# Optimization experiments

Hardware: AMD Instinct MI355X
Metric: run time of the kernel (lower is better)

The kernel has to match this reference:

```python
import jax, jax.numpy as jnp
import numpy as np

SEM_ENC_DIM = 1024
SENT_HIDDEN_DIM = 1024
ATT_DIM = 512

def setup_inputs() -> dict:
    key = jax.random.key(0)
    ks = jax.random.split(key, 8)
    B, L = 64, 2048
    s = lambda d: 1.0 / np.sqrt(d)
    return {
        "sem_enc_output": jax.random.normal(ks[0], (B, L, SEM_ENC_DIM), dtype=jnp.float32),
        "dec_hidden_state": jax.random.normal(ks[1], (B, SENT_HIDDEN_DIM), dtype=jnp.float32),
        "W_enc": jax.random.uniform(ks[2], (SEM_ENC_DIM, ATT_DIM), jnp.float32, -s(SEM_ENC_DIM), s(SEM_ENC_DIM)),
        "b_enc": jax.random.uniform(ks[3], (ATT_DIM,), jnp.float32, -s(SEM_ENC_DIM), s(SEM_ENC_DIM)),
        "W_dec": jax.random.uniform(ks[4], (SENT_HIDDEN_DIM, ATT_DIM), jnp.float32, -s(SENT_HIDDEN_DIM), s(SENT_HIDDEN_DIM)),
        "b_dec": jax.random.uniform(ks[5], (ATT_DIM,), jnp.float32, -s(SENT_HIDDEN_DIM), s(SENT_HIDDEN_DIM)),
        "W_full": jax.random.uniform(ks[6], (ATT_DIM, 1), jnp.float32, -s(ATT_DIM), s(ATT_DIM)),
        "b_full": jax.random.uniform(ks[7], (1,), jnp.float32, -s(ATT_DIM), s(ATT_DIM)),
    }

def reference(sem_enc_output, dec_hidden_state, W_enc, b_enc, W_dec, b_dec, W_full, b_full):
    # enc projection: [B, L, att_dim]
    enc_proj = jnp.einsum('ble,ea->bla', sem_enc_output, W_enc) + b_enc
    # dec projection: [B, att_dim]
    dec_proj = dec_hidden_state @ W_dec + b_dec
    # broadcast add + tanh: [B, L, att_dim]
    joined = jnp.tanh(enc_proj + dec_proj[:, None, :])
    # scoring: [B, L]
    scores = (jnp.einsum('bla,a->bl', joined, W_full[:, 0]) + b_full[0])
    att_scores = jax.nn.softmax(scores, axis=1)
    # weighted sum over L of the PROJECTED encoder output (matches torch code)
    att_output = jnp.einsum('bl,bla->ba', att_scores, enc_proj)
    return (att_output, att_scores)
```

## Files before the change

### kernel.cpp

```cpp
#include <hip/hip_runtime.h>
#include <hip/hip_bf16.h>
#include <cstdint>
#include <cstddef>

#define BB   64
#define LL   2048
#define ED   1024
#define AD   512
#define BM   128
#define NCH  (LL / BM)
#define NBURST 8

typedef short  short8  __attribute__((ext_vector_type(8)));
typedef float  f32x4   __attribute__((ext_vector_type(4)));

__device__ __forceinline__ unsigned short f2bf(float x) {
  unsigned u = __float_as_uint(x);
  u += 0x7FFFu + ((u >> 16) & 1u);
  return (unsigned short)(u >> 16);
}

__device__ __forceinline__ short8 cvt8(f32x4 lo, f32x4 hi) {
  union { short8 s; unsigned u[4]; } r;
  asm("v_cvt_pk_bf16_f32 %0, %1, %2" : "=v"(r.u[0]) : "v"(lo[0]), "v"(lo[1]));
  asm("v_cvt_pk_bf16_f32 %0, %1, %2" : "=v"(r.u[1]) : "v"(lo[2]), "v"(lo[3]));
  asm("v_cvt_pk_bf16_f32 %0, %1, %2" : "=v"(r.u[2]) : "v"(hi[0]), "v"(hi[1]));
  asm("v_cvt_pk_bf16_f32 %0, %1, %2" : "=v"(r.u[3]) : "v"(hi[2]), "v"(hi[3]));
  return r.s;
}

#define GLOAD_LDS16(gp, lp)                                                        \
  __builtin_amdgcn_global_load_lds(                                                \
      (const __attribute__((address_space(1))) unsigned int*)(gp),                 \
      (__attribute__((address_space(3))) unsigned int*)(lp), 16, 0, 0)

__global__ __launch_bounds__(512) void prep_kernel(
    const float* __restrict__ W_enc, const float* __restrict__ dec,
    const float* __restrict__ W_dec, const float* __restrict__ b_dec,
    unsigned short* __restrict__ Wb, float* __restrict__ dp) {
  const int blk = blockIdx.x, t = threadIdx.x;
  if (blk < BB) {
    const float* drow = dec + blk * ED;
    float a0 = 0.f, a1 = 0.f, a2 = 0.f, a3 = 0.f;
    for (int k = 0; k < ED; k += 4) {
      a0 = fmaf(drow[k],     W_dec[(k)     * AD + t], a0);
      a1 = fmaf(drow[k + 1], W_dec[(k + 1) * AD + t], a1);
      a2 = fmaf(drow[k + 2], W_dec[(k + 2) * AD + t], a2);
      a3 = fmaf(drow[k + 3], W_dec[(k + 3) * AD + t], a3);
    }
    dp[blk * AD + t] = (a0 + a1) + (a2 + a3) + b_dec[t];
  } else {
    const int base = (blk - BB) * 4096;
#pragma unroll
    for (int ii = 0; ii < 8; ii++) {
      const int o    = base + ii * 512 + t;
      const int ks   = o >> 14;
      const int cblk = (o >> 9) & 31;
      const int kg   = (o >> 7) & 3;
      const int r    = (o >> 3) & 15;
      const int j    = o & 7;
      const int k    = ks * 32 + kg * 8 + j;
      const int c    = cblk * 16 + r;
      Wb[o] = f2bf(W_enc[k * AD + c]);
    }
  }
}

__global__ __launch_bounds__(512, 2) void fused_kernel(
    const float* __restrict__ sem, const unsigned short* __restrict__ Wb,
    const float* __restrict__ dp, const float* __restrict__ b_enc,
    const float* __restrict__ Wf,
    float* __restrict__ raw_scores,
    float* __restrict__ ws_ms, float* __restrict__ ws_o) {

  __shared__ float Alds[2][16384];

  const int t    = threadIdx.x;
  const int lane = t & 63;
  const int wave = t >> 6;
  const int wm   = wave >> 2;
  const int wn   = wave & 3;
  const int b    = blockIdx.y;
  const int chunk= blockIdx.x;
  const int l0   = chunk * BM;

  const int trow = t >> 5;
  const int su   = (t & 31) ^ (trow & 7);
  const float* asrc = sem + ((size_t)(b * LL + l0 + trow)) * ED + su * 4;

  const int arow = lane & 15;
  const int akg  = lane >> 4;
  const int lxor = lane & 7;
  const int akg2 = akg * 2;
  const int arbase = (wm * 64 + arow) * 128;

  const unsigned short* wbbase = Wb + wn * 4096 + lane * 8;

  f32x4 acc[4][8];
#pragma unroll
  for (int i = 0; i < 4; i++)
#pragma unroll
    for (int j = 0; j < 8; j++) acc[i][j] = (f32x4)0.f;

#define STAGE_A(g, nb)                                                             \
  _Pragma("unroll")                                                                \
  for (int j = 0; j < 8; j++)                                                      \
    GLOAD_LDS16(asrc + (size_t)j * 16384 + (g) * 128, &Alds[nb][j * 2048 + t * 4]);

  STAGE_A(0, 0);
  asm volatile("s_waitcnt vmcnt(0)" ::: "memory");
  __builtin_amdgcn_sched_barrier(0);
  __builtin_amdgcn_s_barrier();

  for (int g = 0; g < NBURST; g++) {
    const int cb = g & 1;
    if (g + 1 < NBURST) STAGE_A(g + 1, cb ^ 1);
    __builtin_amdgcn_sched_barrier(0);
    const unsigned short* wbg = wbbase + g * 65536;
#pragma unroll
    for (int ks4 = 0; ks4 < 4; ks4++) {
      short8 bv[8];
#pragma unroll
      for (int nf = 0; nf < 8; nf++)
        bv[nf] = *(const short8*)(wbg + ks4 * 16384 + nf * 512);
      short8 av[4];
#pragma unroll
      for (int mf = 0; mf < 4; mf++) {
        const int s0 = (ks4 * 8 + akg2) ^ lxor;
        const int s1 = (ks4 * 8 + akg2 + 1) ^ lxor;
        f32x4 lo = *(const f32x4*)&Alds[cb][arbase + mf * 2048 + s0 * 4];
        f32x4 hi = *(const f32x4*)&Alds[cb][arbase + mf * 2048 + s1 * 4];
        av[mf] = cvt8(lo, hi);
      }
      __builtin_amdgcn_s_setprio(1);
#pragma unroll
      for (int mf = 0; mf < 4; mf++)
#pragma unroll
        for (int nf = 0; nf < 8; nf++)
          acc[mf][nf] = __builtin_amdgcn_mfma_f32_16x16x32_bf16(av[mf], bv[nf], acc[mf][nf], 0, 0, 0);
      __builtin_amdgcn_s_setprio(0);
    }
    asm volatile("s_waitcnt vmcnt(0) lgkmcnt(0)" ::: "memory");
    __builtin_amdgcn_sched_barrier(0);
    __builtin_amdgcn_s_barrier();
  }
#undef STAGE_A

  float* eb = (float*)&Alds[0][0];
  float (*sc_part)[4]   = (float (*)[4])eb;
  float* scores_lds     = eb + 512;
  float* weight         = eb + 640;
  float (*o_lds)[AD]    = (float (*)[AD])(eb + 768);
  float* bcv            = eb + 1792;

  float dpv[8], wfv[8], bev[8];
#pragma unroll
  for (int nf = 0; nf < 8; nf++) {
    const int c = wn * 128 + nf * 16 + arow;
    dpv[nf] = dp[b * AD + c];
    wfv[nf] = Wf[c];
    bev[nf] = b_enc[c];
  }
#pragma unroll
  for (int mf = 0; mf < 4; mf++) {
#pragma unroll
    for (int r = 0; r < 4; r++) {
      float p = 0.f;
#pragma unroll
      for (int nf = 0; nf < 8; nf++) {
        float e = acc[mf][nf][r] + bev[nf];
        acc[mf][nf][r] = e;
        float x = e + dpv[nf];
        float ex = __expf(2.f * x);
        float th = 1.f - 2.f / (ex + 1.f);
        p = fmaf(th, wfv[nf], p);
      }
      p += __shfl_xor(p, 1); p += __shfl_xor(p, 2);
      p += __shfl_xor(p, 4); p += __shfl_xor(p, 8);
      if (arow == 0) sc_part[wm * 64 + mf * 16 + akg * 4 + r][wn] = p;
    }
  }
  __syncthreads();

  if (t < BM) {
    float s = sc_part[t][0] + sc_part[t][1] + sc_part[t][2] + sc_part[t][3];
    scores_lds[t] = s;
    raw_scores[(size_t)b * LL + l0 + t] = s;
  }
  __syncthreads();
  if (t < 64) {
    float m = fmaxf(scores_lds[t], scores_lds[t + 64]);
#pragma unroll
    for (int off = 1; off < 64; off <<= 1) m = fmaxf(m, __shfl_xor(m, off));
    if (t == 0) bcv[0] = m;
  }
  __syncthreads();
  const float m_c = bcv[0];
  if (t < BM) weight[t] = __expf(scores_lds[t] - m_c);
  __syncthreads();
  if (t < 64) {
    float s = weight[t] + weight[t + 64];
#pragma unroll
    for (int off = 1; off < 64; off <<= 1) s += __shfl_xor(s, off);
    if (t == 0) bcv[1] = s;
  }

  float wv[4][4];
#pragma unroll
  for (int mf = 0; mf < 4; mf++)
#pragma unroll
    for (int r = 0; r < 4; r++) wv[mf][r] = weight[wm * 64 + mf * 16 + akg * 4 + r];
#pragma unroll
  for (int nf = 0; nf < 8; nf++) {
    float cp = 0.f;
#pragma unroll
    for (int mf = 0; mf < 4; mf++)
#pragma unroll
      for (int r = 0; r < 4; r++) cp = fmaf(wv[mf][r], acc[mf][nf][r], cp);
    cp += __shfl_xor(cp, 16);
    cp += __shfl_xor(cp, 32);
    if (lane < 16) o_lds[wm][wn * 128 + nf * 16 + lane] = cp;
  }
  __syncthreads();
  if (t < AD)
    ws_o[((size_t)b * NCH + chunk) * AD + t] = o_lds[0][t] + o_lds[1][t];
  if (t == 0) {
    ws_ms[(b * NCH + chunk) * 2]     = m_c;
    ws_ms[(b * NCH + chunk) * 2 + 1] = bcv[1];
  }
}

__global__ __launch_bounds__(256) void finalize_kernel(
    const float* __restrict__ ws_ms, const float* __restrict__ ws_o,
    float* __restrict__ out0, float* __restrict__ outS) {
  const int b = blockIdx.x, t = threadIdx.x;
  float ms[NCH], ss[NCH];
  float M = -1e30f;
#pragma unroll
  for (int i = 0; i < NCH; i++) {
    ms[i] = ws_ms[(b * NCH + i) * 2];
    ss[i] = ws_ms[(b * NCH + i) * 2 + 1];
    M = fmaxf(M, ms[i]);
  }
  float S = 0.f, w[NCH];
#pragma unroll
  for (int i = 0; i < NCH; i++) { w[i] = __expf(ms[i] - M); S = fmaf(ss[i], w[i], S); }
  const float invS = 1.f / S;
  for (int c = t; c < AD; c += 256) {
    float a = 0.f;
#pragma unroll
    for (int i = 0; i < NCH; i++) a = fmaf(ws_o[((size_t)b * NCH + i) * AD + c], w[i], a);
    out0[b * AD + c] = a * invS;
  }
  for (int l = t; l < LL; l += 256) {
    float r = outS[(size_t)b * LL + l];
    outS[(size_t)b * LL + l] = __expf(r - M) * invS;
  }
}

extern "C" void kernel_launch(void* const* d_in, const int* in_sizes, int n_in,
                              void* d_out, int out_size, void* d_ws, size_t ws_size,
                              hipStream_t stream) {
  const float* sem    = (const float*)d_in[0];
  const float* dec    = (const float*)d_in[1];
  const float* W_enc  = (const float*)d_in[2];
  const float* b_enc  = (const float*)d_in[3];
  const float* W_dec  = (const float*)d_in[4];
  const float* b_dec  = (const float*)d_in[5];
  const float* W_full = (const float*)d_in[6];

  float* out0 = (float*)d_out;
  float* outS = out0 + BB * AD;

  char* ws = (char*)d_ws;
  unsigned short* Wb = (unsigned short*)ws;
  float* dpw   = (float*)(ws + (1 << 20));
  float* ws_ms = (float*)(ws + (1 << 20) + (128 << 10));
  float* ws_o  = (float*)(ws + (1 << 20) + (136 << 10));

  prep_kernel<<<BB + 128, 512, 0, stream>>>(W_enc, dec, W_dec, b_dec, Wb, dpw);
  dim3 g1(NCH, BB);
  fused_kernel<<<g1, 512, 0, stream>>>(sem, Wb, dpw, b_enc, W_full, outS, ws_ms, ws_o);
  finalize_kernel<<<BB, 256, 0, stream>>>(ws_ms, ws_o, out0, outS);
}
```

Baseline: 277.0 us.

## Restructure GEMM main loop into a 32-step K pipeline with LDS-staged bf16 A/B

Replaces the 8-burst loop, which staged fp32 A tiles into LDS and read B directly from global, with a 32-step K loop. A is loaded into registers, converted to bf16 and written to a double-buffered LDS tile. B is staged into a triple-buffered LDS ring via direct global-to-LDS loads. Each K step is split into four MFMA phases separated by barriers, so that loads for step k+2 overlap compute. The aim is to cut global B reads per wave and shrink the LDS footprint, at the cost of many more barriers per step and a more complex buffer rotation schedule.

```diff
diff --git a/kernel.cpp b/kernel.cpp
--- a/kernel.cpp
+++ b/kernel.cpp
@@ -9,7 +9,7 @@
 #define AD   512
 #define BM   128
 #define NCH  (LL / BM)
-#define NBURST 8
+#define NT   32
 
 typedef short  short8  __attribute__((ext_vector_type(8)));
 typedef float  f32x4   __attribute__((ext_vector_type(4)));
@@ -73,7 +73,8 @@
     float* __restrict__ raw_scores,
     float* __restrict__ ws_ms, float* __restrict__ ws_o) {
 
-  __shared__ float Alds[2][16384];
+  __shared__ unsigned short Ab[2][4096];
+  __shared__ unsigned short Bb[3][16384];
 
   const int t    = threadIdx.x;
   const int lane = t & 63;
@@ -84,17 +85,16 @@
   const int chunk= blockIdx.x;
   const int l0   = chunk * BM;
 
-  const int trow = t >> 5;
-  const int su   = (t & 31) ^ (trow & 7);
-  const float* asrc = sem + ((size_t)(b * LL + l0 + trow)) * ED + su * 4;
+  const int srow = t >> 2;
+  const int skg  = t & 3;
+  const float* aptr = sem + ((size_t)(b * LL + l0 + srow)) * ED + skg * 8;
+  const unsigned short* bsrc = Wb + t * 8;
+  const int awr = (srow >> 4) * 512 + skg * 128 + (srow & 15) * 8;
 
   const int arow = lane & 15;
   const int akg  = lane >> 4;
-  const int lxor = lane & 7;
-  const int akg2 = akg * 2;
-  const int arbase = (wm * 64 + arow) * 128;
-
-  const unsigned short* wbbase = Wb + wn * 4096 + lane * 8;
+  const int afr  = wm * 2048 + lane * 8;
+  const int bfr  = wn * 4096 + lane * 8;
 
   f32x4 acc[4][8];
 #pragma unroll
@@ -102,51 +102,104 @@
 #pragma unroll
     for (int j = 0; j < 8; j++) acc[i][j] = (f32x4)0.f;
 
-#define STAGE_A(g, nb)                                                             \
-  _Pragma("unroll")                                                                \
-  for (int j = 0; j < 8; j++)                                                      \
-    GLOAD_LDS16(asrc + (size_t)j * 16384 + (g) * 128, &Alds[nb][j * 2048 + t * 4]);
-
-  STAGE_A(0, 0);
-  asm volatile("s_waitcnt vmcnt(0)" ::: "memory");
+#pragma unroll
+  for (int i = 0; i < 4; i++)
+    GLOAD_LDS16(bsrc + i * 4096, &Bb[0][i * 4096 + t * 8]);
+#pragma unroll
+  for (int i = 0; i < 4; i++)
+    GLOAD_LDS16(bsrc + 16384 + i * 4096, &Bb[1][i * 4096 + t * 8]);
+  f32x4 tA0 = *(const f32x4*)(aptr);
+  f32x4 tA1 = *(const f32x4*)(aptr + 4);
+  f32x4 qA0 = *(const f32x4*)(aptr + 32);
+  f32x4 qA1 = *(const f32x4*)(aptr + 36);
+  f32x4 pA0, pA1;
+  {
+    short8 aw = cvt8(tA0, tA1);
+    *(short8*)&Ab[0][awr] = aw;
+  }
+  asm volatile("s_waitcnt vmcnt(2) lgkmcnt(0)" ::: "memory");
   __builtin_amdgcn_sched_barrier(0);
   __builtin_amdgcn_s_barrier();
 
-  for (int g = 0; g < NBURST; g++) {
-    const int cb = g & 1;
-    if (g + 1 < NBURST) STAGE_A(g + 1, cb ^ 1);
+#define PHASE_MFMA(E, O, bE, bO)                                                   \
+    __builtin_amdgcn_s_setprio(1);                                                 \
+    acc[0][E] = __builtin_amdgcn_mfma_f32_16x16x32_bf16(av0, bE, acc[0][E], 0,0,0);\
+    acc[1][E] = __builtin_amdgcn_mfma_f32_16x16x32_bf16(av1, bE, acc[1][E], 0,0,0);\
+    acc[2][E] = __builtin_amdgcn_mfma_f32_16x16x32_bf16(av2, bE, acc[2][E], 0,0,0);\
+    acc[3][E] = __builtin_amdgcn_mfma_f32_16x16x32_bf16(av3, bE, acc[3][E], 0,0,0);\
+    acc[0][O] = __builtin_amdgcn_mfma_f32_16x16x32_bf16(av0, bO, acc[0][O], 0,0,0);\
+    acc[1][O] = __builtin_amdgcn_mfma_f32_16x16x32_bf16(av1, bO, acc[1][O], 0,0,0);\
+    acc[2][O] = __builtin_amdgcn_mfma_f32_16x16x32_bf16(av2, bO, acc[2][O], 0,0,0);\
+    acc[3][O] = __builtin_amdgcn_mfma_f32_16x16x32_bf16(av3, bO, acc[3][O], 0,0,0);\
+    __builtin_amdgcn_s_setprio(0);
+
+#define BARRIER_LGKM                                                               \
+    __builtin_amdgcn_s_barrier();                                                  \
+    asm volatile("s_waitcnt lgkmcnt(0)" ::: "memory");                             \
     __builtin_amdgcn_sched_barrier(0);
-    const unsigned short* wbg = wbbase + g * 65536;
-#pragma unroll
-    for (int ks4 = 0; ks4 < 4; ks4++) {
-      short8 bv[8];
-#pragma unroll
-      for (int nf = 0; nf < 8; nf++)
-        bv[nf] = *(const short8*)(wbg + ks4 * 16384 + nf * 512);
-      short8 av[4];
-#pragma unroll
-      for (int mf = 0; mf < 4; mf++) {
-        const int s0 = (ks4 * 8 + akg2) ^ lxor;
-        const int s1 = (ks4 * 8 + akg2 + 1) ^ lxor;
-        f32x4 lo = *(const f32x4*)&Alds[cb][arbase + mf * 2048 + s0 * 4];
-        f32x4 hi = *(const f32x4*)&Alds[cb][arbase + mf * 2048 + s1 * 4];
-        av[mf] = cvt8(lo, hi);
-      }
-      __builtin_amdgcn_s_setprio(1);
-#pragma unroll
-      for (int mf = 0; mf < 4; mf++)
-#pragma unroll
-        for (int nf = 0; nf < 8; nf++)
-          acc[mf][nf] = __builtin_amdgcn_mfma_f32_16x16x32_bf16(av[mf], bv[nf], acc[mf][nf], 0, 0, 0);
-      __builtin_amdgcn_s_setprio(0);
-    }
-    asm volatile("s_waitcnt vmcnt(0) lgkmcnt(0)" ::: "memory");
-    __builtin_amdgcn_sched_barrier(0);
-    __builtin_amdgcn_s_barrier();
-  }
-#undef STAGE_A
-
-  float* eb = (float*)&Alds[0][0];
+
+#define ITER(ks, BR, BW, AR, AW, CA0, CA1, LA0, LA1, STG, CVT, VM)                 \
+  {                                                                                \
+                                                                 \
+    short8 av0 = *(const short8*)&Ab[AR][afr];                                     \
+    short8 av1 = *(const short8*)&Ab[AR][afr + 512];                               \
+    short8 av2 = *(const short8*)&Ab[AR][afr + 1024];                              \
+    short8 av3 = *(const short8*)&Ab[AR][afr + 1536];                              \
+    short8 b0 = *(const short8*)&Bb[BR][bfr];                                      \
+    short8 b1 = *(const short8*)&Bb[BR][bfr + 512];                                \
+    if (STG) {                                                                     \
+      GLOAD_LDS16(bsrc + ((ks) + 2) * 16384, &Bb[BW][t * 8]);                      \
+      const float* ap = aptr + ((ks) + 2) * 32;                                    \
+      LA0 = *(const f32x4*)(ap);                                                   \
+      LA1 = *(const f32x4*)(ap + 4);                                               \
+    }                                                                              \
+    BARRIER_LGKM                                                                   \
+    PHASE_MFMA(0, 1, b0, b1)                                                       \
+    __builtin_amdgcn_s_barrier();                                                  \
+                                                                 \
+    short8 b2 = *(const short8*)&Bb[BR][bfr + 1024];                               \
+    short8 b3 = *(const short8*)&Bb[BR][bfr + 1536];                               \
+    if (STG) GLOAD_LDS16(bsrc + ((ks) + 2) * 16384 + 4096, &Bb[BW][4096 + t * 8]); \
+    BARRIER_LGKM                                                                   \
+    PHASE_MFMA(2, 3, b2, b3)                                                       \
+    __builtin_amdgcn_s_barrier();                                                  \
+                                                                 \
+    short8 b4 = *(const short8*)&Bb[BR][bfr + 2048];                               \
+    short8 b5 = *(const short8*)&Bb[BR][bfr + 2560];                               \
+    if (STG) GLOAD_LDS16(bsrc + ((ks) + 2) * 16384 + 8192, &Bb[BW][8192 + t * 8]); \
+    BARRIER_LGKM                                                                   \
+    PHASE_MFMA(4, 5, b4, b5)                                                       \
+    __builtin_amdgcn_s_barrier();                                                  \
+                                                                 \
+    short8 b6 = *(const short8*)&Bb[BR][bfr + 3072];                               \
+    short8 b7 = *(const short8*)&Bb[BR][bfr + 3584];                               \
+    if (STG) GLOAD_LDS16(bsrc + ((ks) + 2) * 16384 + 12288, &Bb[BW][12288 + t * 8]);\
+    if (CVT) {                                                                     \
+      short8 aw = cvt8(CA0, CA1);          \
+      *(short8*)&Ab[AW][awr] = aw;                                                 \
+    }                                                                              \
+    BARRIER_LGKM                                                                   \
+    PHASE_MFMA(6, 7, b6, b7)                                                       \
+    asm volatile("s_waitcnt vmcnt(" #VM ")" ::: "memory");                         \
+    __builtin_amdgcn_sched_barrier(0);                                             \
+    __builtin_amdgcn_s_barrier();                                                  \
+  }
+
+  for (int base = 0; base < 30; base += 6) {
+    ITER(base + 0, 0, 2, 0, 1, qA0, qA1, pA0, pA1, 1, 1, 6)
+    ITER(base + 1, 1, 0, 1, 0, pA0, pA1, qA0, qA1, 1, 1, 6)
+    ITER(base + 2, 2, 1, 0, 1, qA0, qA1, pA0, pA1, 1, 1, 6)
+    ITER(base + 3, 0, 2, 1, 0, pA0, pA1, qA0, qA1, 1, 1, 6)
+    ITER(base + 4, 1, 0, 0, 1, qA0, qA1, pA0, pA1, 1, 1, 6)
+    ITER(base + 5, 2, 1, 1, 0, pA0, pA1, qA0, qA1, 1, 1, 6)
+  }
+  ITER(30, 0, 0, 0, 1, qA0, qA1, pA0, pA1, 0, 1, 0)
+  ITER(31, 1, 0, 1, 0, pA0, pA1, qA0, qA1, 0, 0, 0)
+#undef ITER
+#undef BARRIER_LGKM
+#undef PHASE_MFMA
+
+  float* eb = (float*)&Bb[0][0];
   float (*sc_part)[4]   = (float (*)[4])eb;
   float* scores_lds     = eb + 512;
   float* weight         = eb + 640;
```

New measurement: 314.8 us. 13.7% more time.

## Stage A tile via registers as bf16 in LDS with per-k-step double buffering

Applied to the files above, without the earlier changes.

Replaces the large fp32 direct-to-LDS staging of the activation tile (two 64KB buffers, 8 bursts of 128 k) with a register-prefetched pipeline. Each k-step of 32 loads fp32 from global into registers two steps ahead, converts to bf16 once, and writes it into a small double-buffered LDS tile laid out in MFMA fragment order. The epilogue gets its own small LDS array, which cuts LDS use sharply and could allow more occupancy. W fragments are loaded with nontemporal hints. The cost is a barrier every 32-wide k-step instead of every 128, and latency hiding that depends on register prefetch.

```diff
diff --git a/kernel.cpp b/kernel.cpp
--- a/kernel.cpp
+++ b/kernel.cpp
@@ -9,7 +9,7 @@
 #define AD   512
 #define BM   128
 #define NCH  (LL / BM)
-#define NBURST 8
+#define KST  32
 
 typedef short  short8  __attribute__((ext_vector_type(8)));
 typedef float  f32x4   __attribute__((ext_vector_type(4)));
@@ -73,7 +73,8 @@
     float* __restrict__ raw_scores,
     float* __restrict__ ws_ms, float* __restrict__ ws_o) {
 
-  __shared__ float Alds[2][16384];
+  __shared__ unsigned short Ab[2][4096];
+  __shared__ float epi[1800];
 
   const int t    = threadIdx.x;
   const int lane = t & 63;
@@ -84,17 +85,15 @@
   const int chunk= blockIdx.x;
   const int l0   = chunk * BM;
 
-  const int trow = t >> 5;
-  const int su   = (t & 31) ^ (trow & 7);
-  const float* asrc = sem + ((size_t)(b * LL + l0 + trow)) * ED + su * 4;
+  const int srow = t >> 2;
+  const int skg  = t & 3;
+  const float* aptr = sem + ((size_t)(b * LL + l0 + srow)) * ED + skg * 8;
+  const int awr = (srow >> 4) * 512 + skg * 128 + (srow & 15) * 8;
 
   const int arow = lane & 15;
   const int akg  = lane >> 4;
-  const int lxor = lane & 7;
-  const int akg2 = akg * 2;
-  const int arbase = (wm * 64 + arow) * 128;
-
-  const unsigned short* wbbase = Wb + wn * 4096 + lane * 8;
+  const int afr  = wm * 2048 + lane * 8;
+  const unsigned short* wbb = Wb + wn * 4096 + lane * 8;
 
   f32x4 acc[4][8];
 #pragma unroll
@@ -102,56 +101,68 @@
 #pragma unroll
     for (int j = 0; j < 8; j++) acc[i][j] = (f32x4)0.f;
 
-#define STAGE_A(g, nb)                                                             \
-  _Pragma("unroll")                                                                \
-  for (int j = 0; j < 8; j++)                                                      \
-    GLOAD_LDS16(asrc + (size_t)j * 16384 + (g) * 128, &Alds[nb][j * 2048 + t * 4]);
-
-  STAGE_A(0, 0);
-  asm volatile("s_waitcnt vmcnt(0)" ::: "memory");
+  f32x4 pA0 = *(const f32x4*)(aptr);
+  f32x4 pA1 = *(const f32x4*)(aptr + 4);
+  f32x4 qA0 = *(const f32x4*)(aptr + 32);
+  f32x4 qA1 = *(const f32x4*)(aptr + 36);
+  *(short8*)&Ab[0][awr] = cvt8(pA0, pA1);
+  asm volatile("s_waitcnt lgkmcnt(0)" ::: "memory");
   __builtin_amdgcn_sched_barrier(0);
   __builtin_amdgcn_s_barrier();
 
-  for (int g = 0; g < NBURST; g++) {
-    const int cb = g & 1;
-    if (g + 1 < NBURST) STAGE_A(g + 1, cb ^ 1);
-    __builtin_amdgcn_sched_barrier(0);
-    const unsigned short* wbg = wbbase + g * 65536;
-#pragma unroll
-    for (int ks4 = 0; ks4 < 4; ks4++) {
-      short8 bv[8];
-#pragma unroll
-      for (int nf = 0; nf < 8; nf++)
-        bv[nf] = *(const short8*)(wbg + ks4 * 16384 + nf * 512);
-      short8 av[4];
-#pragma unroll
-      for (int mf = 0; mf < 4; mf++) {
-        const int s0 = (ks4 * 8 + akg2) ^ lxor;
-        const int s1 = (ks4 * 8 + akg2 + 1) ^ lxor;
-        f32x4 lo = *(const f32x4*)&Alds[cb][arbase + mf * 2048 + s0 * 4];
-        f32x4 hi = *(const f32x4*)&Alds[cb][arbase + mf * 2048 + s1 * 4];
-        av[mf] = cvt8(lo, hi);
-      }
-      __builtin_amdgcn_s_setprio(1);
-#pragma unroll
-      for (int mf = 0; mf < 4; mf++)
-#pragma unroll
-        for (int nf = 0; nf < 8; nf++)
-          acc[mf][nf] = __builtin_amdgcn_mfma_f32_16x16x32_bf16(av[mf], bv[nf], acc[mf][nf], 0, 0, 0);
-      __builtin_amdgcn_s_setprio(0);
-    }
-    asm volatile("s_waitcnt vmcnt(0) lgkmcnt(0)" ::: "memory");
-    __builtin_amdgcn_sched_barrier(0);
-    __builtin_amdgcn_s_barrier();
-  }
-#undef STAGE_A
-
-  float* eb = (float*)&Alds[0][0];
-  float (*sc_part)[4]   = (float (*)[4])eb;
-  float* scores_lds     = eb + 512;
-  float* weight         = eb + 640;
-  float (*o_lds)[AD]    = (float (*)[AD])(eb + 768);
-  float* bcv            = eb + 1792;
+#define ITER(ks, CA0, CA1, LA0, LA1)                                               \
+  {                                                                                \
+    const int cb = (ks) & 1, nb = ((ks) + 1) & 1;                                  \
+    const unsigned short* wq = wbb + (size_t)(ks) * 16384;                         \
+    short8 bv0 = __builtin_nontemporal_load((const short8*)(wq));                  \
+    short8 bv1 = __builtin_nontemporal_load((const short8*)(wq + 512));            \
+    short8 bv2 = __builtin_nontemporal_load((const short8*)(wq + 1024));           \
+    short8 bv3 = __builtin_nontemporal_load((const short8*)(wq + 1536));           \
+    short8 bv4 = __builtin_nontemporal_load((const short8*)(wq + 2048));           \
+    short8 bv5 = __builtin_nontemporal_load((const short8*)(wq + 2560));           \
+    short8 bv6 = __builtin_nontemporal_load((const short8*)(wq + 3072));           \
+    short8 bv7 = __builtin_nontemporal_load((const short8*)(wq + 3584));           \
+    if ((ks) + 2 < KST) {                                                          \
+      const float* ap = aptr + ((ks) + 2) * 32;                                    \
+      LA0 = *(const f32x4*)(ap);                                                   \
+      LA1 = *(const f32x4*)(ap + 4);                                               \
+    }                                                                              \
+    __builtin_amdgcn_sched_barrier(0);     \
+    if ((ks) + 1 < KST)                                                            \
+      *(short8*)&Ab[nb][awr] = cvt8(CA0, CA1);                                     \
+    short8 av[4];                                                                  \
+    _Pragma("unroll")                                                              \
+    for (int mf = 0; mf < 4; mf++)                                                 \
+      av[mf] = *(const short8*)&Ab[cb][afr + mf * 512];                            \
+    __builtin_amdgcn_s_setprio(1);                                                 \
+    _Pragma("unroll")                                                              \
+    for (int mf = 0; mf < 4; mf++) {                                               \
+      acc[mf][0] = __builtin_amdgcn_mfma_f32_16x16x32_bf16(av[mf], bv0, acc[mf][0], 0, 0, 0); \
+      acc[mf][1] = __builtin_amdgcn_mfma_f32_16x16x32_bf16(av[mf], bv1, acc[mf][1], 0, 0, 0); \
+      acc[mf][2] = __builtin_amdgcn_mfma_f32_16x16x32_bf16(av[mf], bv2, acc[mf][2], 0, 0, 0); \
+      acc[mf][3] = __builtin_amdgcn_mfma_f32_16x16x32_bf16(av[mf], bv3, acc[mf][3], 0, 0, 0); \
+      acc[mf][4] = __builtin_amdgcn_mfma_f32_16x16x32_bf16(av[mf], bv4, acc[mf][4], 0, 0, 0); \
+      acc[mf][5] = __builtin_amdgcn_mfma_f32_16x16x32_bf16(av[mf], bv5, acc[mf][5], 0, 0, 0); \
+      acc[mf][6] = __builtin_amdgcn_mfma_f32_16x16x32_bf16(av[mf], bv6, acc[mf][6], 0, 0, 0); \
+      acc[mf][7] = __builtin_amdgcn_mfma_f32_16x16x32_bf16(av[mf], bv7, acc[mf][7], 0, 0, 0); \
+    }                                                                              \
+    __builtin_amdgcn_s_setprio(0);                                                 \
+    asm volatile("s_waitcnt lgkmcnt(0)" ::: "memory");                             \
+    __builtin_amdgcn_sched_barrier(0);                                             \
+    __builtin_amdgcn_s_barrier();                                                  \
+  }
+
+  for (int kk = 0; kk < KST; kk += 2) {
+    ITER(kk,     qA0, qA1, pA0, pA1);
+    ITER(kk + 1, pA0, pA1, qA0, qA1);
+  }
+#undef ITER
+
+  float (*sc_part)[4]   = (float (*)[4])epi;
+  float* scores_lds     = epi + 512;
+  float* weight         = epi + 640;
+  float (*o_lds)[AD]    = (float (*)[AD])(epi + 768);
+  float* bcv            = epi + 1792;
 
   float dpv[8], wfv[8], bev[8];
 #pragma unroll
```

Result: slower. 362.0 us (+30.7%).
